# Optimization experiments

Measured on AMD Instinct MI355X. Metric: run time of the kernel, lower is better.

The kernel has to match this reference:

```python
import jax, jax.numpy as jnp
import numpy as np

B, L, D_MODEL, D_INNER, P = 4, 16384, 256, 512, 64  # P = d_state, conj_sym=False
STEP_RESCALE = 1.0


def setup_inputs() -> dict:
    key = jax.random.key(0)
    ks = jax.random.split(key, 11)
    # projections (bias=False)
    W_in = jax.random.normal(ks[0], (D_MODEL, 2 * D_INNER), jnp.float32) * (1.0 / np.sqrt(D_MODEL))
    W_out = jax.random.normal(ks[1], (D_INNER, D_MODEL), jnp.float32) * (1.0 / np.sqrt(D_INNER))
    # diagonal SSM params: Lambda = A_real + i*A_imag, HiPPO-like (negative real part)
    A_real = -0.5 * jnp.ones((P,), jnp.float32) - jax.random.uniform(ks[2], (P,), jnp.float32)
    A_imag = jnp.pi * jnp.arange(P, dtype=jnp.float32) * (jax.random.uniform(ks[3], (P,), jnp.float32) * 0.1 + 0.95)
    B_re = jax.random.normal(ks[4], (P, D_INNER), jnp.float32) * (1.0 / np.sqrt(P))
    B_im = jax.random.normal(ks[5], (P, D_INNER), jnp.float32) * (1.0 / np.sqrt(P))
    C_re = jax.random.normal(ks[6], (D_INNER, P), jnp.float32) * (1.0 / np.sqrt(D_INNER))
    C_im = jax.random.normal(ks[7], (D_INNER, P), jnp.float32) * (1.0 / np.sqrt(D_INNER))
    D = jax.random.normal(ks[8], (D_INNER,), jnp.float32)
    # dt ~ loguniform[dt_min, dt_max]; inv_dt = softplus^{-1}(dt) = dt + log(-expm1(-dt))
    dt = jnp.exp(jax.random.uniform(ks[9], (P,), jnp.float32) * (np.log(0.1) - np.log(0.001)) + np.log(0.001))
    dt = jnp.clip(dt, 1e-4, None)
    inv_dt = dt + jnp.log(-jnp.expm1(-dt))
    x = jax.random.normal(ks[10], (B, L, D_MODEL), jnp.float32)
    return {"x": x, "W_in": W_in, "W_out": W_out, "A_real": A_real, "A_imag": A_imag,
            "B_re": B_re, "B_im": B_im, "C_re": C_re, "C_im": C_im, "D": D, "inv_dt": inv_dt}


def _binop(e1, e2):
    a1, b1 = e1
    a2, b2 = e2
    return a2 * a1, a2 * b1 + b2


def reference(x, W_in, W_out, A_real, A_imag, B_re, B_im, C_re, C_im, D, inv_dt):
    # in_proj + gate split
    x_and_res = x @ W_in                       # (b, l, 2*d_inner)
    u, res = jnp.split(x_and_res, 2, axis=-1)
    u = jax.nn.silu(u)                         # (b, l, d_inner)
    # bilinear discretization of diagonal SSM
    A = A_real + 1j * A_imag                   # (P,)
    dt = STEP_RESCALE * jax.nn.softplus(inv_dt)  # (P,)
    BL = 1.0 / (1.0 - (dt / 2.0) * A)
    dA = BL * (1.0 + (dt / 2.0) * A)           # (P,)
    dB = (BL * dt)[:, None] * (B_re + 1j * B_im)  # (P, d_inner)
    # drive: Bu_t = dB @ u_t
    Bu = u.astype(dA.dtype) @ dB.T             # (b, l, P) complex
    # parallel (associative) scan of h_t = dA*h_{t-1} + Bu_t  (h_0 = 0)
    elems = (jnp.broadcast_to(dA, Bu.shape), Bu)
    _, h = jax.lax.associative_scan(_binop, elems, axis=1)  # (b, l, P)
    C = C_re + 1j * C_im                       # (d_inner, P)
    y = jnp.real(h @ C.T) + D * u              # (b, l, d_inner), + skip D*u
    y = y * jax.nn.silu(res)
    return y @ W_out                           # (b, l, d_model)
```

## Files before the change

### kernel.cpp

```cpp
#include <hip/hip_runtime.h>
#include <math.h>

#define NTOK 65536
#define LSEQ 16384
#define GCH 64
#define NCH 256

typedef __attribute__((ext_vector_type(8))) short short8v;
typedef __attribute__((ext_vector_type(4))) float f32x4;
typedef unsigned short u16;

__device__ __forceinline__ u16 f2bf(float f) {
  unsigned u = __float_as_uint(f);
  return (u16)((u + 0x7FFFu + ((u >> 16) & 1u)) >> 16);
}
__device__ __forceinline__ float bf2f(u16 b) {
  return __uint_as_float(((unsigned)b) << 16);
}
__device__ __forceinline__ unsigned cvtpk_bf16(float lo, float hi) {
  unsigned r;
  asm("v_cvt_pk_bf16_f32 %0, %1, %2" : "=v"(r) : "v"(lo), "v"(hi));
  return r;
}
__device__ __forceinline__ float silu_f(float v) {
  return v * __builtin_amdgcn_rcpf(1.f + __expf(-v));
}
__device__ __forceinline__ void gld16(const u16* g, u16* l) {
  __builtin_amdgcn_global_load_lds((const __attribute__((address_space(1))) void*)g,
                                   (__attribute__((address_space(3))) void*)l, 16, 0, 0);
}

#define WAITV2 asm volatile("s_waitcnt vmcnt(2) lgkmcnt(0)" ::: "memory")
#define WAITV0 asm volatile("s_waitcnt vmcnt(0) lgkmcnt(0)" ::: "memory")
#define BARRAW asm volatile("s_barrier" ::: "memory")

__global__ void setup_scalar_k(const float* __restrict__ A_real, const float* __restrict__ A_imag,
                               const float* __restrict__ inv_dt,
                               float2* __restrict__ dAf, float2* __restrict__ fvec,
                               float2* __restrict__ powt) {
  int p = threadIdx.x;
  if (p >= 64) return;
  double ar = (double)A_real[p], ai = (double)A_imag[p];
  double dt = log1p(exp((double)inv_dt[p]));
  double zr = 0.5 * dt * ar, zi = 0.5 * dt * ai;
  double d1r = 1.0 - zr;
  double den = d1r * d1r + zi * zi;
  double blr = d1r / den, bli = zi / den;
  double nr = 1.0 + zr, ni = zi;
  double dar = blr * nr - bli * ni;
  double dai = blr * ni + bli * nr;
  dAf[p] = make_float2((float)dar, (float)dai);
  fvec[p] = make_float2((float)(blr * dt), (float)(bli * dt));
  double cr = 1.0, ci = 0.0;
  for (int k = 0; k <= GCH; ++k) {
    powt[p * (GCH + 1) + k] = make_float2((float)cr, (float)ci);
    double t = cr * dar - ci * dai;
    ci = cr * dai + ci * dar;
    cr = t;
  }
}

__global__ void setup_tables_k(const float* __restrict__ B_re, const float* __restrict__ B_im,
                               const float* __restrict__ C_re, const float* __restrict__ C_im,
                               const float* __restrict__ W_in, const float* __restrict__ W_out,
                               const float2* __restrict__ fvec,
                               u16* __restrict__ WinT, u16* __restrict__ dBn,
                               u16* __restrict__ Ccb, u16* __restrict__ WoutT) {
  int idx = blockIdx.x * blockDim.x + threadIdx.x;
  int stride = gridDim.x * blockDim.x;
  for (int i = idx; i < 1024 * 256; i += stride) {
    int n = i >> 8, k = i & 255;
    WinT[i] = f2bf(W_in[k * 1024 + n]);
  }
  for (int i = idx; i < 128 * 512; i += stride) {
    int p = i >> 9, d = i & 511;
    float2 f = fvec[p & 63];
    float br = B_re[(p & 63) * 512 + d], bi = B_im[(p & 63) * 512 + d];
    float v = (p < 64) ? (f.x * br - f.y * bi) : (f.x * bi + f.y * br);
    dBn[i] = f2bf(v);
  }
  for (int i = idx; i < 512 * 128; i += stride) {
    int d = i >> 7, k = i & 127;
    float v = (k < 64) ? C_re[d * 64 + k] : -C_im[d * 64 + (k - 64)];
    Ccb[i] = f2bf(v);
  }
  for (int i = idx; i < 256 * 512; i += stride) {
    int n = i >> 9, k = i & 511;
    WoutT[i] = f2bf(W_out[k * 256 + n]);
  }
}

__global__ __launch_bounds__(256) void cvt_x_k(const float* __restrict__ x, u16* __restrict__ xb) {
  size_t i = ((size_t)blockIdx.x * blockDim.x + threadIdx.x) * 4;
  size_t stride = (size_t)gridDim.x * blockDim.x * 4;
  const size_t total = (size_t)NTOK * 256;
  for (; i < total; i += stride) {
    float4 v = *(const float4*)(x + i);
    ushort4 o;
    o.x = f2bf(v.x); o.y = f2bf(v.y); o.z = f2bf(v.z); o.w = f2bf(v.w);
    *(ushort4*)(xb + i) = o;
  }
}

template<int MODE, int LOG_NBX, int KDIM>
__global__ __launch_bounds__(512) void mgemm(
    const u16* __restrict__ A, const u16* __restrict__ Bt,
    void* __restrict__ C0, void* __restrict__ C1,
    const float* __restrict__ Dvec) {
  __shared__ u16 As[3][128 * 32];
  __shared__ u16 Bs[3][128 * 32];
  const int tid = threadIdx.x;
  const int w = tid >> 6, l = tid & 63;
  const int wm = w >> 2, wn = w & 3;

  const int lin = blockIdx.x;
  const int cpx = gridDim.x >> 3;
  const int swz = (lin & 7) * cpx + (lin >> 3);
  const int n0 = (swz & ((1 << LOG_NBX) - 1)) * 128;
  const int m0 = (swz >> LOG_NBX) * 128;

  f32x4 acc[4][2] = {};

  const int lr = l >> 2;
  const int sc = (l & 3) ^ ((l >> 3) & 3);
  const u16* gA = A + (size_t)(m0 + w * 16 + lr) * KDIM + sc * 8;
  const u16* gB = Bt + (size_t)(n0 + w * 16 + lr) * KDIM + sc * 8;

  const int fr = l & 15;
  const int kgs = (((l >> 4) ^ (l >> 1)) & 3) * 8;

  constexpr int NT = KDIM / 32;

  auto stage = [&](int buf, int k0) {
    gld16(gA + k0, &As[buf][w * 512]);
    gld16(gB + k0, &Bs[buf][w * 512]);
  };
  auto compute = [&](int buf) {
    short8v af[4], bfr[2];
#pragma unroll
    for (int mi = 0; mi < 4; ++mi)
      af[mi] = *(const short8v*)&As[buf][(wm * 64 + mi * 16 + fr) * 32 + kgs];
#pragma unroll
    for (int ni = 0; ni < 2; ++ni)
      bfr[ni] = *(const short8v*)&Bs[buf][(wn * 32 + ni * 16 + fr) * 32 + kgs];
#pragma unroll
    for (int mi = 0; mi < 4; ++mi)
#pragma unroll
      for (int ni = 0; ni < 2; ++ni)
        acc[mi][ni] = __builtin_amdgcn_mfma_f32_16x16x32_bf16(af[mi], bfr[ni], acc[mi][ni], 0, 0, 0);
  };

  stage(0, 0);
  if (NT > 1) stage(1, 32);
#pragma unroll
  for (int t = 0; t < NT; ++t) {
    if (t + 1 < NT) { WAITV2; } else { WAITV0; }
    BARRAW;
    if (t + 2 < NT) stage((t + 2) % 3, (t + 2) * 32);
    compute(t % 3);
  }

  const int rbase = (l >> 4) * 4;
#pragma unroll
  for (int mi = 0; mi < 4; ++mi) {
#pragma unroll
    for (int ni = 0; ni < 2; ++ni) {
      int gr0 = m0 + wm * 64 + mi * 16 + rbase;
      int gc = n0 + wn * 32 + ni * 16 + fr;
      if (MODE == 0) {
        float s0 = silu_f(acc[mi][ni][0]);
        float s1 = silu_f(acc[mi][ni][1]);
        float s2 = silu_f(acc[mi][ni][2]);
        float s3 = silu_f(acc[mi][ni][3]);
        unsigned p01 = cvtpk_bf16(s0, s1);
        unsigned p23 = cvtpk_bf16(s2, s3);
        u16* Cw = (n0 < 512) ? (u16*)C0 : (u16*)C1;
        int col = gc - ((n0 < 512) ? 0 : 512);
        Cw[(size_t)(gr0 + 0) * 512 + col] = (u16)p01;
        Cw[(size_t)(gr0 + 1) * 512 + col] = (u16)(p01 >> 16);
        Cw[(size_t)(gr0 + 2) * 512 + col] = (u16)p23;
        Cw[(size_t)(gr0 + 3) * 512 + col] = (u16)(p23 >> 16);
      } else if (MODE == 1) {
#pragma unroll
        for (int j = 0; j < 4; ++j)
          ((float*)C0)[(size_t)(gr0 + j) * 128 + gc] = acc[mi][ni][j];
      } else if (MODE == 2) {
        float g[4];
#pragma unroll
        for (int j = 0; j < 4; ++j) {
          size_t r = (size_t)(gr0 + j);
          float uu = bf2f(((const u16*)C0)[r * 512 + gc]);
          float sr = bf2f(((const u16*)C1)[r * 512 + gc]);
          g[j] = (acc[mi][ni][j] + Dvec[gc] * uu) * sr;
        }
        unsigned p01 = cvtpk_bf16(g[0], g[1]);
        unsigned p23 = cvtpk_bf16(g[2], g[3]);
        ((u16*)C1)[(size_t)(gr0 + 0) * 512 + gc] = (u16)p01;
        ((u16*)C1)[(size_t)(gr0 + 1) * 512 + gc] = (u16)(p01 >> 16);
        ((u16*)C1)[(size_t)(gr0 + 2) * 512 + gc] = (u16)p23;
        ((u16*)C1)[(size_t)(gr0 + 3) * 512 + gc] = (u16)(p23 >> 16);
      } else {
#pragma unroll
        for (int j = 0; j < 4; ++j)
          ((float*)C0)[(size_t)(gr0 + j) * 256 + gc] = acc[mi][ni][j];
      }
    }
  }
}

__global__ __launch_bounds__(256) void scan_sum_k(const float* __restrict__ Bu,
                                                  float* __restrict__ carr,
                                                  const float2* __restrict__ dAf) {
  int unit = blockIdx.x * 4 + (threadIdx.x >> 6);
  int p = threadIdx.x & 63;
  int b = unit >> 8, c = unit & 255;
  float2 dA = dAf[p];
  size_t base = ((size_t)b * LSEQ + (size_t)c * GCH) * 128;
  float rr = 0.f, ri = 0.f;
  for (int i0 = 0; i0 < GCH; i0 += 8) {
    float br[8], bi[8];
#pragma unroll
    for (int j = 0; j < 8; ++j) {
      br[j] = Bu[base + (size_t)(i0 + j) * 128 + p];
      bi[j] = Bu[base + (size_t)(i0 + j) * 128 + 64 + p];
    }
#pragma unroll
    for (int j = 0; j < 8; ++j) {
      float nr = fmaf(dA.x, rr, fmaf(-dA.y, ri, br[j]));
      float ni = fmaf(dA.x, ri, fmaf(dA.y, rr, bi[j]));
      rr = nr; ri = ni;
    }
  }
  carr[(size_t)unit * 128 + p] = rr;
  carr[(size_t)unit * 128 + 64 + p] = ri;
}

__global__ void scan_carry_k(const float* __restrict__ carr, float* __restrict__ offc,
                             const float2* __restrict__ powt) {
  int b = threadIdx.x >> 6;
  int p = threadIdx.x & 63;
  float2 dAG = powt[p * (GCH + 1) + GCH];
  float rr = 0.f, ri = 0.f;
  for (int c0 = 0; c0 < NCH; c0 += 8) {
    float er[8], ei[8];
#pragma unroll
    for (int j = 0; j < 8; ++j) {
      size_t crow = (size_t)(b * NCH + c0 + j) * 128;
      er[j] = carr[crow + p];
      ei[j] = carr[crow + 64 + p];
    }
#pragma unroll
    for (int j = 0; j < 8; ++j) {
      size_t orow = (size_t)(b * NCH + c0 + j) * 128;
      offc[orow + p] = rr;
      offc[orow + 64 + p] = ri;
      float nr = fmaf(dAG.x, rr, fmaf(-dAG.y, ri, er[j]));
      float ni = fmaf(dAG.x, ri, fmaf(dAG.y, rr, ei[j]));
      rr = nr; ri = ni;
    }
  }
}

__global__ __launch_bounds__(256) void scan_emit_k(const float* __restrict__ Bu,
                                                   const float* __restrict__ offc,
                                                   u16* __restrict__ hb,
                                                   const float2* __restrict__ dAf) {
  int unit = blockIdx.x * 4 + (threadIdx.x >> 6);
  int p = threadIdx.x & 63;
  int b = unit >> 8, c = unit & 255;
  float2 dA = dAf[p];
  size_t base = ((size_t)b * LSEQ + (size_t)c * GCH) * 128;
  float hr = offc[(size_t)unit * 128 + p];
  float hi = offc[(size_t)unit * 128 + 64 + p];
  for (int i0 = 0; i0 < GCH; i0 += 8) {
    float br[8], bi[8];
#pragma unroll
    for (int j = 0; j < 8; ++j) {
      br[j] = Bu[base + (size_t)(i0 + j) * 128 + p];
      bi[j] = Bu[base + (size_t)(i0 + j) * 128 + 64 + p];
    }
#pragma unroll
    for (int j = 0; j < 8; ++j) {
      float nr = fmaf(dA.x, hr, fmaf(-dA.y, hi, br[j]));
      float ni = fmaf(dA.x, hi, fmaf(dA.y, hr, bi[j]));
      hr = nr; hi = ni;
      hb[base + (size_t)(i0 + j) * 128 + p] = f2bf(hr);
      hb[base + (size_t)(i0 + j) * 128 + 64 + p] = f2bf(hi);
    }
  }
}

extern "C" void kernel_launch(void* const* d_in, const int* in_sizes, int n_in,
                              void* d_out, int out_size, void* d_ws, size_t ws_size,
                              hipStream_t stream) {
  const float* x      = (const float*)d_in[0];
  const float* W_in   = (const float*)d_in[1];
  const float* W_out  = (const float*)d_in[2];
  const float* A_real = (const float*)d_in[3];
  const float* A_imag = (const float*)d_in[4];
  const float* B_re   = (const float*)d_in[5];
  const float* B_im   = (const float*)d_in[6];
  const float* C_re   = (const float*)d_in[7];
  const float* C_im   = (const float*)d_in[8];
  const float* Dv     = (const float*)d_in[9];
  const float* inv_dt = (const float*)d_in[10];

  u16* xb    = (u16*)d_ws;
  u16* u_bf  = xb + (size_t)NTOK * 256;
  u16* sr_bf = u_bf + (size_t)NTOK * 512;
  u16* h_bf  = sr_bf + (size_t)NTOK * 512;
  u16* WinT  = h_bf + (size_t)NTOK * 128;
  u16* dBn   = WinT + 1024 * 256;
  u16* Ccb   = dBn + 128 * 512;
  u16* WoutT = Ccb + 512 * 128;

  float* O    = (float*)d_out;
  float* Bu   = O;
  float* offc = O + 8388608;
  float* carr = O + 8519680;
  float2* powt = (float2*)(O + 8650752);
  float2* dAf  = (float2*)(O + 8659072);
  float2* fvec = (float2*)(O + 8659200);

  setup_scalar_k<<<1, 64, 0, stream>>>(A_real, A_imag, inv_dt, dAf, fvec, powt);
  setup_tables_k<<<256, 256, 0, stream>>>(B_re, B_im, C_re, C_im, W_in, W_out, fvec,
                                          WinT, dBn, Ccb, WoutT);
  cvt_x_k<<<1024, 256, 0, stream>>>(x, xb);

  mgemm<0, 3, 256><<<4096, 512, 0, stream>>>(xb, WinT, u_bf, sr_bf, nullptr);
  mgemm<1, 0, 512><<<512, 512, 0, stream>>>(u_bf, dBn, Bu, nullptr, nullptr);
  scan_sum_k<<<256, 256, 0, stream>>>(Bu, carr, dAf);
  scan_carry_k<<<1, 256, 0, stream>>>(carr, offc, powt);
  scan_emit_k<<<256, 256, 0, stream>>>(Bu, offc, h_bf, dAf);
  mgemm<2, 2, 128><<<2048, 512, 0, stream>>>(h_bf, Ccb, u_bf, sr_bf, Dv);
  mgemm<3, 1, 512><<<1024, 512, 0, stream>>>(sr_bf, WoutT, O, nullptr, nullptr);
}
```

Before: 210.2 us.

## Fuse x fp32 conversion into in_proj GEMM, fold chunk sums into Bu GEMM, widen tiles

The in_proj GEMM now reads fp32 x directly and converts it to bf16 while staging into LDS, which removes the separate cvt_x pass and its bf16 intermediate. The Bu GEMM epilogue computes the per-chunk scan sums from its accumulators using dA powers and cross-lane shuffles, replacing the scan_sum kernel's second read of Bu. The real and imaginary partial carries go to two buffers that scan_carry adds together. The other GEMMs move to 1024-thread blocks with 128x256 tiles and dedicated loader waves. In exchange, the fp32 A path uses register staging with only double buffering, and the larger blocks may lower occupancy.

```diff
diff --git a/kernel.cpp b/kernel.cpp
--- a/kernel.cpp
+++ b/kernel.cpp
@@ -31,6 +31,7 @@
 }
 
 #define WAITV2 asm volatile("s_waitcnt vmcnt(2) lgkmcnt(0)" ::: "memory")
+#define WAITV1 asm volatile("s_waitcnt vmcnt(1) lgkmcnt(0)" ::: "memory")
 #define WAITV0 asm volatile("s_waitcnt vmcnt(0) lgkmcnt(0)" ::: "memory")
 #define BARRAW asm volatile("s_barrier" ::: "memory")
 
@@ -90,50 +91,63 @@
   }
 }
 
-__global__ __launch_bounds__(256) void cvt_x_k(const float* __restrict__ x, u16* __restrict__ xb) {
-  size_t i = ((size_t)blockIdx.x * blockDim.x + threadIdx.x) * 4;
-  size_t stride = (size_t)gridDim.x * blockDim.x * 4;
-  const size_t total = (size_t)NTOK * 256;
-  for (; i < total; i += stride) {
-    float4 v = *(const float4*)(x + i);
-    ushort4 o;
-    o.x = f2bf(v.x); o.y = f2bf(v.y); o.z = f2bf(v.z); o.w = f2bf(v.w);
-    *(ushort4*)(xb + i) = o;
-  }
-}
-
-template<int MODE, int LOG_NBX, int KDIM>
-__global__ __launch_bounds__(512) void mgemm(
-    const u16* __restrict__ A, const u16* __restrict__ Bt,
+template<int MODE, int LOG_NBX, int KDIM, int AFP32>
+__global__ __launch_bounds__(1024) void mgemm2(
+    const void* __restrict__ Ain, const u16* __restrict__ Bt,
     void* __restrict__ C0, void* __restrict__ C1,
     const float* __restrict__ Dvec) {
-  __shared__ u16 As[3][128 * 32];
-  __shared__ u16 Bs[3][128 * 32];
+  constexpr int NBUF = AFP32 ? 2 : 3;
+  constexpr int NT = KDIM / 32;
+  __shared__ u16 As[NBUF][128 * 32];
+  __shared__ u16 Bs[NBUF][256 * 32];
   const int tid = threadIdx.x;
   const int w = tid >> 6, l = tid & 63;
-  const int wm = w >> 2, wn = w & 3;
+  const int wm = w >> 3, wn = w & 7;
+  const bool isA = (w < 8);
 
   const int lin = blockIdx.x;
   const int cpx = gridDim.x >> 3;
   const int swz = (lin & 7) * cpx + (lin >> 3);
-  const int n0 = (swz & ((1 << LOG_NBX) - 1)) * 128;
+  const int n0 = (swz & ((1 << LOG_NBX) - 1)) * 256;
   const int m0 = (swz >> LOG_NBX) * 128;
 
   f32x4 acc[4][2] = {};
-
-  const int lr = l >> 2;
-  const int sc = (l & 3) ^ ((l >> 3) & 3);
-  const u16* gA = A + (size_t)(m0 + w * 16 + lr) * KDIM + sc * 8;
-  const u16* gB = Bt + (size_t)(n0 + w * 16 + lr) * KDIM + sc * 8;
 
   const int fr = l & 15;
   const int kgs = (((l >> 4) ^ (l >> 1)) & 3) * 8;
-
-  constexpr int NT = KDIM / 32;
-
-  auto stage = [&](int buf, int k0) {
-    gld16(gA + k0, &As[buf][w * 512]);
-    gld16(gB + k0, &Bs[buf][w * 512]);
+  const int sr = l >> 2;
+  const int scl = l & 3;
+  const int scs = scl ^ ((l >> 3) & 3);
+
+  const float* gA32 = nullptr;
+  const u16* gA16 = nullptr;
+  const u16* gB = nullptr;
+  if (isA) {
+    int row = w * 16 + sr;
+    if (AFP32) gA32 = (const float*)Ain + (size_t)(m0 + row) * KDIM + scl * 8;
+    else       gA16 = (const u16*)Ain + (size_t)(m0 + row) * KDIM + scs * 8;
+  } else {
+    int row = (w - 8) * 16 + sr;
+    gB = Bt + (size_t)(n0 + row) * KDIM + scs * 8;
+  }
+
+  float4 ra0, ra1;
+  auto loadA = [&](int k0) {
+    ra0 = *(const float4*)(gA32 + k0);
+    ra1 = *(const float4*)(gA32 + k0 + 4);
+  };
+  auto writeA = [&](int buf) {
+    unsigned q0 = cvtpk_bf16(ra0.x, ra0.y), q1 = cvtpk_bf16(ra0.z, ra0.w);
+    unsigned q2 = cvtpk_bf16(ra1.x, ra1.y), q3 = cvtpk_bf16(ra1.z, ra1.w);
+    int row = w * 16 + sr;
+    *(uint4*)&As[buf][row * 32 + scs * 8] = make_uint4(q0, q1, q2, q3);
+  };
+  auto stageB = [&](int buf, int k0) {
+    gld16(gB + k0, &Bs[buf][(w - 8) * 512]);
+    gld16(gB + k0 + (size_t)128 * KDIM, &Bs[buf][(w - 8) * 512 + 4096]);
+  };
+  auto stageA16 = [&](int buf, int k0) {
+    gld16(gA16 + k0, &As[buf][w * 512]);
   };
   auto compute = [&](int buf) {
     short8v af[4], bfr[2];
@@ -150,14 +164,41 @@
         acc[mi][ni] = __builtin_amdgcn_mfma_f32_16x16x32_bf16(af[mi], bfr[ni], acc[mi][ni], 0, 0, 0);
   };
 
-  stage(0, 0);
-  if (NT > 1) stage(1, 32);
-#pragma unroll
-  for (int t = 0; t < NT; ++t) {
-    if (t + 1 < NT) { WAITV2; } else { WAITV0; }
-    BARRAW;
-    if (t + 2 < NT) stage((t + 2) % 3, (t + 2) * 32);
-    compute(t % 3);
+  if (AFP32) {
+    if (isA) {
+      loadA(0);
+      asm volatile("s_waitcnt vmcnt(0)" ::: "memory");
+      writeA(0);
+    } else {
+      stageB(0, 0);
+    }
+    __syncthreads();
+#pragma unroll
+    for (int t = 0; t < NT; ++t) {
+      if (t + 1 < NT) {
+        if (isA) loadA((t + 1) * 32);
+        else     stageB((t + 1) & 1, (t + 1) * 32);
+      }
+      compute(t & 1);
+      if (t + 1 < NT && isA) {
+        asm volatile("s_waitcnt vmcnt(0)" ::: "memory");
+        writeA((t + 1) & 1);
+      }
+      __syncthreads();
+    }
+  } else {
+    if (isA) stageA16(0, 0); else stageB(0, 0);
+    if (isA) stageA16(1, 32); else stageB(1, 32);
+#pragma unroll
+    for (int t = 0; t < NT; ++t) {
+      if (t + 1 < NT) { if (isA) { WAITV1; } else { WAITV2; } } else { WAITV0; }
+      BARRAW;
+      if (t + 2 < NT) {
+        if (isA) stageA16((t + 2) % 3, (t + 2) * 32);
+        else     stageB((t + 2) % 3, (t + 2) * 32);
+      }
+      compute(t % 3);
+    }
   }
 
   const int rbase = (l >> 4) * 4;
@@ -180,18 +221,14 @@
         Cw[(size_t)(gr0 + 1) * 512 + col] = (u16)(p01 >> 16);
         Cw[(size_t)(gr0 + 2) * 512 + col] = (u16)p23;
         Cw[(size_t)(gr0 + 3) * 512 + col] = (u16)(p23 >> 16);
-      } else if (MODE == 1) {
-#pragma unroll
-        for (int j = 0; j < 4; ++j)
-          ((float*)C0)[(size_t)(gr0 + j) * 128 + gc] = acc[mi][ni][j];
       } else if (MODE == 2) {
         float g[4];
 #pragma unroll
         for (int j = 0; j < 4; ++j) {
           size_t r = (size_t)(gr0 + j);
           float uu = bf2f(((const u16*)C0)[r * 512 + gc]);
-          float sr = bf2f(((const u16*)C1)[r * 512 + gc]);
-          g[j] = (acc[mi][ni][j] + Dvec[gc] * uu) * sr;
+          float sr2 = bf2f(((const u16*)C1)[r * 512 + gc]);
+          g[j] = (acc[mi][ni][j] + Dvec[gc] * uu) * sr2;
         }
         unsigned p01 = cvtpk_bf16(g[0], g[1]);
         unsigned p23 = cvtpk_bf16(g[2], g[3]);
@@ -208,35 +245,107 @@
   }
 }
 
-__global__ __launch_bounds__(256) void scan_sum_k(const float* __restrict__ Bu,
-                                                  float* __restrict__ carr,
-                                                  const float2* __restrict__ dAf) {
-  int unit = blockIdx.x * 4 + (threadIdx.x >> 6);
-  int p = threadIdx.x & 63;
-  int b = unit >> 8, c = unit & 255;
-  float2 dA = dAf[p];
-  size_t base = ((size_t)b * LSEQ + (size_t)c * GCH) * 128;
-  float rr = 0.f, ri = 0.f;
-  for (int i0 = 0; i0 < GCH; i0 += 8) {
-    float br[8], bi[8];
-#pragma unroll
-    for (int j = 0; j < 8; ++j) {
-      br[j] = Bu[base + (size_t)(i0 + j) * 128 + p];
-      bi[j] = Bu[base + (size_t)(i0 + j) * 128 + 64 + p];
-    }
-#pragma unroll
-    for (int j = 0; j < 8; ++j) {
-      float nr = fmaf(dA.x, rr, fmaf(-dA.y, ri, br[j]));
-      float ni = fmaf(dA.x, ri, fmaf(dA.y, rr, bi[j]));
-      rr = nr; ri = ni;
-    }
-  }
-  carr[(size_t)unit * 128 + p] = rr;
-  carr[(size_t)unit * 128 + 64 + p] = ri;
-}
-
-__global__ void scan_carry_k(const float* __restrict__ carr, float* __restrict__ offc,
-                             const float2* __restrict__ powt) {
+__global__ __launch_bounds__(512) void k2_bu_carry(
+    const u16* __restrict__ A, const u16* __restrict__ Bt,
+    float* __restrict__ Bu, float* __restrict__ carr, float* __restrict__ carr2,
+    const float2* __restrict__ dAf, const float2* __restrict__ powt) {
+  constexpr int KDIM = 512;
+  constexpr int NT = KDIM / 32;
+  __shared__ u16 As[3][128 * 32];
+  __shared__ u16 Bs[3][128 * 32];
+  const int tid = threadIdx.x;
+  const int w = tid >> 6, l = tid & 63;
+  const int wm = w >> 2, wn = w & 3;
+
+  const int lin = blockIdx.x;
+  const int cpx = gridDim.x >> 3;
+  const int swz = (lin & 7) * cpx + (lin >> 3);
+  const int m0 = swz * 128;
+
+  f32x4 acc[4][2] = {};
+
+  const int lr = l >> 2;
+  const int sc = (l & 3) ^ ((l >> 3) & 3);
+  const u16* gA = A + (size_t)(m0 + w * 16 + lr) * KDIM + sc * 8;
+  const u16* gB = Bt + (size_t)(w * 16 + lr) * KDIM + sc * 8;
+
+  const int fr = l & 15;
+  const int kgs = (((l >> 4) ^ (l >> 1)) & 3) * 8;
+
+  auto stage = [&](int buf, int k0) {
+    gld16(gA + k0, &As[buf][w * 512]);
+    gld16(gB + k0, &Bs[buf][w * 512]);
+  };
+  auto compute = [&](int buf) {
+    short8v af[4], bfr[2];
+#pragma unroll
+    for (int mi = 0; mi < 4; ++mi)
+      af[mi] = *(const short8v*)&As[buf][(wm * 64 + mi * 16 + fr) * 32 + kgs];
+#pragma unroll
+    for (int ni = 0; ni < 2; ++ni)
+      bfr[ni] = *(const short8v*)&Bs[buf][(wn * 32 + ni * 16 + fr) * 32 + kgs];
+#pragma unroll
+    for (int mi = 0; mi < 4; ++mi)
+#pragma unroll
+      for (int ni = 0; ni < 2; ++ni)
+        acc[mi][ni] = __builtin_amdgcn_mfma_f32_16x16x32_bf16(af[mi], bfr[ni], acc[mi][ni], 0, 0, 0);
+  };
+
+  stage(0, 0);
+  stage(1, 32);
+#pragma unroll
+  for (int t = 0; t < NT; ++t) {
+    if (t + 1 < NT) { WAITV2; } else { WAITV0; }
+    BARRAW;
+    if (t + 2 < NT) stage((t + 2) % 3, (t + 2) * 32);
+    compute(t % 3);
+  }
+
+  const int lg = l >> 4;
+  const int rbase = lg * 4;
+#pragma unroll
+  for (int mi = 0; mi < 4; ++mi)
+#pragma unroll
+    for (int ni = 0; ni < 2; ++ni) {
+      int gr0 = m0 + wm * 64 + mi * 16 + rbase;
+      int gc = wn * 32 + ni * 16 + fr;
+#pragma unroll
+      for (int j = 0; j < 4; ++j)
+        Bu[(size_t)(gr0 + j) * 128 + gc] = acc[mi][ni][j];
+    }
+  const int cu = (m0 >> 6) + wm;
+#pragma unroll
+  for (int ni = 0; ni < 2; ++ni) {
+    int gc = wn * 32 + ni * 16 + fr;
+    int p = gc & 63;
+    float2 dA = dAf[p];
+    float sre = 0.f, sim = 0.f;
+#pragma unroll
+    for (int mi = 0; mi < 4; ++mi) {
+      float tr = 0.f, ti = 0.f;
+#pragma unroll
+      for (int j = 0; j < 4; ++j) {
+        float v = acc[mi][ni][j];
+        float nr = fmaf(dA.x, tr, fmaf(-dA.y, ti, v));
+        float nim = fmaf(dA.x, ti, dA.y * tr);
+        tr = nr; ti = nim;
+      }
+      float2 wg = powt[p * (GCH + 1) + 60 - lg * 4 - 16 * mi];
+      sre = fmaf(wg.x, tr, fmaf(-wg.y, ti, sre));
+      sim = fmaf(wg.x, ti, fmaf(wg.y, tr, sim));
+    }
+    sre += __shfl_xor(sre, 16); sim += __shfl_xor(sim, 16);
+    sre += __shfl_xor(sre, 32); sim += __shfl_xor(sim, 32);
+    if (lg == 0) {
+      size_t crow = (size_t)cu * 128;
+      if (gc < 64) { carr[crow + p] = sre;  carr[crow + 64 + p] = sim; }
+      else         { carr2[crow + p] = -sim; carr2[crow + 64 + p] = sre; }
+    }
+  }
+}
+
+__global__ void scan_carry_k(const float* __restrict__ carr, const float* __restrict__ carr2,
+                             float* __restrict__ offc, const float2* __restrict__ powt) {
   int b = threadIdx.x >> 6;
   int p = threadIdx.x & 63;
   float2 dAG = powt[p * (GCH + 1) + GCH];
@@ -246,8 +355,8 @@
 #pragma unroll
     for (int j = 0; j < 8; ++j) {
       size_t crow = (size_t)(b * NCH + c0 + j) * 128;
-      er[j] = carr[crow + p];
-      ei[j] = carr[crow + 64 + p];
+      er[j] = carr[crow + p] + carr2[crow + p];
+      ei[j] = carr[crow + 64 + p] + carr2[crow + 64 + p];
     }
 #pragma unroll
     for (int j = 0; j < 8; ++j) {
@@ -305,8 +414,7 @@
   const float* Dv     = (const float*)d_in[9];
   const float* inv_dt = (const float*)d_in[10];
 
-  u16* xb    = (u16*)d_ws;
-  u16* u_bf  = xb + (size_t)NTOK * 256;
+  u16* u_bf  = (u16*)d_ws;
   u16* sr_bf = u_bf + (size_t)NTOK * 512;
   u16* h_bf  = sr_bf + (size_t)NTOK * 512;
   u16* WinT  = h_bf + (size_t)NTOK * 128;
@@ -318,20 +426,19 @@
   float* Bu   = O;
   float* offc = O + 8388608;
   float* carr = O + 8519680;
-  float2* powt = (float2*)(O + 8650752);
-  float2* dAf  = (float2*)(O + 8659072);
-  float2* fvec = (float2*)(O + 8659200);
+  float* car2 = O + 8650752;
+  float2* powt = (float2*)(O + 8781824);
+  float2* dAf  = (float2*)(O + 8790144);
+  float2* fvec = (float2*)(O + 8790272);
 
   setup_scalar_k<<<1, 64, 0, stream>>>(A_real, A_imag, inv_dt, dAf, fvec, powt);
   setup_tables_k<<<256, 256, 0, stream>>>(B_re, B_im, C_re, C_im, W_in, W_out, fvec,
                                           WinT, dBn, Ccb, WoutT);
-  cvt_x_k<<<1024, 256, 0, stream>>>(x, xb);
-
-  mgemm<0, 3, 256><<<4096, 512, 0, stream>>>(xb, WinT, u_bf, sr_bf, nullptr);
-  mgemm<1, 0, 512><<<512, 512, 0, stream>>>(u_bf, dBn, Bu, nullptr, nullptr);
-  scan_sum_k<<<256, 256, 0, stream>>>(Bu, carr, dAf);
-  scan_carry_k<<<1, 256, 0, stream>>>(carr, offc, powt);
+
+  mgemm2<0, 2, 256, 1><<<2048, 1024, 0, stream>>>(x, WinT, u_bf, sr_bf, nullptr);
+  k2_bu_carry<<<512, 512, 0, stream>>>(u_bf, dBn, Bu, carr, car2, dAf, powt);
+  scan_carry_k<<<1, 256, 0, stream>>>(carr, car2, offc, powt);
   scan_emit_k<<<256, 256, 0, stream>>>(Bu, offc, h_bf, dAf);
-  mgemm<2, 2, 128><<<2048, 512, 0, stream>>>(h_bf, Ccb, u_bf, sr_bf, Dv);
-  mgemm<3, 1, 512><<<1024, 512, 0, stream>>>(sr_bf, WoutT, O, nullptr, nullptr);
-}
+  mgemm2<2, 1, 128, 0><<<1024, 1024, 0, stream>>>(h_bf, Ccb, u_bf, sr_bf, Dv);
+  mgemm2<3, 0, 512, 0><<<512, 1024, 0, stream>>>(sr_bf, WoutT, O, nullptr, nullptr);
+}
```

Result: slower. 239.2 us (+13.8%).
